# Kernel optimization log

Hardware: AMD Instinct MI355X
Metric: run time of the kernel (lower is better)

The kernel has to match this reference:

```python
import jax, jax.numpy as jnp
import numpy as np

NEG = -1e12


def setup_inputs() -> dict:
    key = jax.random.key(0)
    ks = jax.random.split(key, 6)
    B, S, D, H = 32, 2048, 1024, 1024  # batch, seq, dec/enc dim, hidden
    last_state = jax.random.normal(ks[0], (B, D), dtype=jnp.float32)
    enc_outputs = jax.random.normal(ks[1], (B, S, D), dtype=jnp.float32)
    attn_masks = jax.random.randint(ks[2], (B, S), 0, 2, dtype=jnp.int32)
    W = jax.random.normal(ks[3], (H, 2 * D), dtype=jnp.float32) * 0.02
    b = jax.random.normal(ks[4], (H,), dtype=jnp.float32) * 0.02
    V = jax.random.normal(ks[5], (H,), dtype=jnp.float32)
    return {"last_state": last_state, "enc_outputs": enc_outputs,
            "attn_masks": attn_masks, "W": W, "b": b, "V": V}


def reference(last_state, enc_outputs, attn_masks, W, b, V):
    # Split W to avoid materializing the [B,S,2D] concat:
    # concat([h, e]) @ W.T == h @ Wh.T + e @ We.T
    D = last_state.shape[-1]
    Wh, We = W[:, :D], W[:, D:]
    # hidden part: [B,H], broadcast over seq
    h_part = jnp.einsum('bd,hd->bh', last_state, Wh)  # [B,H]
    e_part = jnp.einsum('bsd,hd->bsh', enc_outputs, We)  # [B,S,H]
    sim = jnp.tanh(h_part[:, None, :] + e_part + b)  # [B,S,H]
    scores = jnp.einsum('bsh,h->bs', sim, V)  # [B,S]
    scores = jnp.where(attn_masks != 1, jnp.float32(NEG), scores)
    attn_weights = jax.nn.softmax(scores, axis=1)  # [B,S]
    context = jnp.einsum('bs,bsd->bd', attn_weights, enc_outputs)  # [B,D]
    return context, attn_weights, scores
```

## Files before the change

### kernel.cpp

```cpp
#include <hip/hip_runtime.h>
#include <math.h>
#include <stdint.h>

#define B_ 32
#define S_ 2048
#define D_ 1024
#define H_ 1024
#define NEGV -1000000000000.0f

typedef __attribute__((ext_vector_type(8))) short bf16x8;
typedef __attribute__((ext_vector_type(8))) _Float16 f16x8;
typedef __attribute__((ext_vector_type(4))) float f32x4;

static __device__ __forceinline__ unsigned short f2bf(float x) {
    union { float f; unsigned u; } v; v.f = x;
    unsigned r = v.u + 0x7FFF + ((v.u >> 16) & 1);
    return (unsigned short)(r >> 16);
}
static __device__ __forceinline__ float bf2f(unsigned short h) {
    union { float f; unsigned u; } v; v.u = ((unsigned)h) << 16; return v.f;
}
static __device__ __forceinline__ unsigned short f2h(float x) {
    _Float16 h = (_Float16)x; unsigned short u;
    __builtin_memcpy(&u, &h, 2); return u;
}
static __device__ __forceinline__ float h2f(unsigned short u) {
    _Float16 h; __builtin_memcpy(&h, &u, 2); return (float)h;
}
static __device__ __forceinline__ float tanh_fast(float x) {
    float e = __expf(2.f * x);
    return 1.f - 2.f / (e + 1.f);
}
static __device__ __forceinline__ void gl_lds16(unsigned short* lds, const unsigned short* g) {
    __builtin_amdgcn_global_load_lds(
        (const __attribute__((address_space(1))) unsigned int*)(const void*)g,
        (__attribute__((address_space(3))) unsigned int*)(void*)lds,
        16, 0, 0);
}

__global__ __launch_bounds__(256) void k_W_f16(const float* __restrict__ W,
                                               unsigned short* __restrict__ out) {
    int idx = blockIdx.x * 256 + threadIdx.x;
    int h = idx >> 7, kc = idx & 127;
    const float* src = W + (size_t)h * (2 * D_) + D_ + kc * 8;
    float4 a = *(const float4*)src;
    float4 c4 = *(const float4*)(src + 4);
    float v[8] = {a.x, a.y, a.z, a.w, c4.x, c4.y, c4.z, c4.w};
    unsigned short t[8];
#pragma unroll
    for (int j = 0; j < 8; ++j) t[j] = f2h(v[j]);
    uint4 w;
    w.x = t[0] | ((unsigned)t[1] << 16); w.y = t[2] | ((unsigned)t[3] << 16);
    w.z = t[4] | ((unsigned)t[5] << 16); w.w = t[6] | ((unsigned)t[7] << 16);
    int g = kc >> 3, cc = kc & 7;
    int dst = g * 64 + ((cc ^ (h & 7)) << 3);
    *(uint4*)(out + (size_t)h * D_ + dst) = w;
}

__global__ __launch_bounds__(256) void k_enc_f16(const float* __restrict__ enc,
                                                 unsigned short* __restrict__ out) {
    size_t gid = (size_t)blockIdx.x * 256 + threadIdx.x;
    size_t row = gid >> 7;
    int kc = (int)(gid & 127);
    const float* src = enc + row * D_ + kc * 8;
    float4 a = *(const float4*)src;
    float4 c4 = *(const float4*)(src + 4);
    float v[8] = {a.x, a.y, a.z, a.w, c4.x, c4.y, c4.z, c4.w};
    unsigned short t[8];
#pragma unroll
    for (int j = 0; j < 8; ++j) t[j] = f2h(v[j]);
    uint4 w;
    w.x = t[0] | ((unsigned)t[1] << 16); w.y = t[2] | ((unsigned)t[3] << 16);
    w.z = t[4] | ((unsigned)t[5] << 16); w.w = t[6] | ((unsigned)t[7] << 16);
    int g = kc >> 3, cc = kc & 7;
    int dst = g * 64 + ((cc ^ ((int)row & 7)) << 3);
    *(uint4*)(out + row * D_ + dst) = w;
}

__global__ __launch_bounds__(256) void k_hpart(const float* __restrict__ ls,
                                               const float* __restrict__ W,
                                               float* __restrict__ hp) {
    int bh = blockIdx.x * 256 + threadIdx.x;
    int b = bh >> 10, h = bh & 1023;
    const float* lsr = ls + b * D_;
    const float* wr  = W + (size_t)h * (2 * D_);
    float acc = 0.f;
#pragma unroll 4
    for (int d = 0; d < D_; d += 4) {
        float4 a = *(const float4*)(lsr + d);
        float4 w = *(const float4*)(wr + d);
        acc += a.x * w.x + a.y * w.y + a.z * w.z + a.w * w.w;
    }
    hp[bh] = acc;
}

__global__ __launch_bounds__(512, 2) void k_scores_f16(
    const unsigned short* __restrict__ ench,
    const unsigned short* __restrict__ Wf16,
    const float* __restrict__ hp, const float* __restrict__ bias,
    const float* __restrict__ V, float* __restrict__ spart)
{
    extern __shared__ unsigned short smem[];
    unsigned short* smemA = smem;
    unsigned short* smemB = smem + 32768;

    const int tid  = threadIdx.x;
    const int lane = tid & 63, wid = tid >> 6;
    const int wm = wid >> 2, wn = wid & 3;
    const int l15 = lane & 15, lhi = lane >> 4;

    const int bid  = blockIdx.x;
    const int wgid = (bid & 7) * 128 + (bid >> 3);
    const int mt = wgid >> 2, nt = wgid & 3;
    const int m0 = mt * 256;
    const int nt256 = nt * 256;
    const int b = m0 >> 11;

    const size_t aoff = (size_t)(m0 + wid * 16 + (lane >> 3)) * D_ + (lane & 7) * 8;
    const size_t boff = (size_t)(nt256 + wid * 16 + (lane >> 3)) * D_ + (lane & 7) * 8;
    const int ldsw = wid * 1024;

    f32x4 acc[8][4];
#pragma unroll
    for (int i = 0; i < 8; ++i)
#pragma unroll
        for (int j = 0; j < 4; ++j)
            acc[i][j] = (f32x4){0.f, 0.f, 0.f, 0.f};

    const int swz = l15 & 7;

#define STAGE_A(SLOT, HALF, KOFS) do {                                              \
    unsigned short* d_ = &smemA[(SLOT) * 16384 + (HALF) * 8192 + ldsw];             \
    const unsigned short* s_ = ench + aoff + (size_t)(HALF) * 131072 + (KOFS);      \
    gl_lds16(d_, s_);                                                               \
    gl_lds16(d_ + 512, s_ + 8192);                                                  \
} while (0)
#define STAGE_B(SLOT, HALF, KOFS) do {                                              \
    unsigned short* d_ = &smemB[(SLOT) * 16384 + (HALF) * 8192 + ldsw];             \
    const unsigned short* s_ = Wf16 + boff + (size_t)(HALF) * 131072 + (KOFS);      \
    gl_lds16(d_, s_);                                                               \
    gl_lds16(d_ + 512, s_ + 8192);                                                  \
} while (0)

#define LDA(AR, CUR, MH, KS) do {                                                   \
    _Pragma("unroll")                                                               \
    for (int fi_ = 0; fi_ < 4; ++fi_) {                                             \
        int row_ = wm * 128 + (MH) * 64 + fi_ * 16 + l15;                           \
        int ch_  = ((KS) * 4 + lhi) ^ swz;                                          \
        AR[fi_] = *(const f16x8*)&smemA[(CUR) * 16384 + row_ * 64 + ch_ * 8];       \
    }                                                                               \
} while (0)
#define LDB(BR, CUR, KS) do {                                                       \
    _Pragma("unroll")                                                               \
    for (int fi_ = 0; fi_ < 4; ++fi_) {                                             \
        int row_ = wn * 64 + fi_ * 16 + l15;                                        \
        int ch_  = ((KS) * 4 + lhi) ^ swz;                                          \
        BR[fi_] = *(const f16x8*)&smemB[(CUR) * 16384 + row_ * 64 + ch_ * 8];       \
    }                                                                               \
} while (0)
#define MFMA16(AR, BR, MH) do {                                                     \
    __builtin_amdgcn_s_setprio(1);                                                  \
    _Pragma("unroll")                                                               \
    for (int fi_ = 0; fi_ < 4; ++fi_)                                               \
    _Pragma("unroll")                                                               \
        for (int fj_ = 0; fj_ < 4; ++fj_)                                           \
            acc[(MH) * 4 + fi_][fj_] = __builtin_amdgcn_mfma_f32_16x16x32_f16(      \
                AR[fi_], BR[fj_], acc[(MH) * 4 + fi_][fj_], 0, 0, 0);               \
    __builtin_amdgcn_s_setprio(0);                                                  \
} while (0)

    STAGE_B(0, 0, 0);
    STAGE_B(0, 1, 0);
    STAGE_A(0, 0, 0);
    STAGE_A(0, 1, 0);
    __syncthreads();

    f16x8 a[4], bk[4];
#pragma unroll 1
    for (int t = 0; t < 16; ++t) {
        const int cur = t & 1, nxt = cur ^ 1;

        if (t < 15) {
            const int kofs = (t + 1) * 64;
            STAGE_B(nxt, 0, kofs);
            STAGE_B(nxt, 1, kofs);
            STAGE_A(nxt, 0, kofs);
            STAGE_A(nxt, 1, kofs);
        }

#pragma unroll
        for (int ks = 0; ks < 2; ++ks) {
            LDB(bk, cur, ks);
            LDA(a, cur, 0, ks);
            MFMA16(a, bk, 0);
            LDA(a, cur, 1, ks);
            MFMA16(a, bk, 1);
        }

        __syncthreads();
    }

    float hb[4], vv[4];
#pragma unroll
    for (int fn = 0; fn < 4; ++fn) {
        int h = nt256 + wn * 64 + fn * 16 + l15;
        hb[fn] = hp[b * H_ + h] + bias[h];
        vv[fn] = V[h];
    }
    float* s_red = (float*)smem;
#pragma unroll
    for (int fm = 0; fm < 8; ++fm)
#pragma unroll
        for (int rg = 0; rg < 4; ++rg) {
            float rs = 0.f;
#pragma unroll
            for (int fn = 0; fn < 4; ++fn)
                rs += tanh_fast(acc[fm][fn][rg] + hb[fn]) * vv[fn];
            rs += __shfl_xor(rs, 1, 16);
            rs += __shfl_xor(rs, 2, 16);
            rs += __shfl_xor(rs, 4, 16);
            rs += __shfl_xor(rs, 8, 16);
            if (l15 == 0)
                s_red[wid * 128 + fm * 16 + lhi * 4 + rg] = rs;
        }
    __syncthreads();
    if (tid < 256) {
        int wmr = tid >> 7, rr = tid & 127;
        float v = s_red[(wmr * 4 + 0) * 128 + rr] + s_red[(wmr * 4 + 1) * 128 + rr]
                + s_red[(wmr * 4 + 2) * 128 + rr] + s_red[(wmr * 4 + 3) * 128 + rr];
        spart[(size_t)nt * 65536 + m0 + tid] = v;
    }
#undef STAGE_A
#undef STAGE_B
#undef LDA
#undef LDB
#undef MFMA16
}

__global__ __launch_bounds__(256) void k_softmax_fold(const float* __restrict__ spart,
                                                      const int* __restrict__ mask,
                                                      float* __restrict__ scores_out,
                                                      float* __restrict__ weights) {
    __shared__ float red[8];
    int b = blockIdx.x, tid = threadIdx.x;
    float vals[8];
    float mx = -INFINITY;
#pragma unroll
    for (int i = 0; i < 8; ++i) {
        int m = b * S_ + tid + i * 256;
        float s = spart[m] + spart[65536 + m] + spart[131072 + m] + spart[196608 + m];
        s = (mask[m] == 1) ? s : NEGV;
        scores_out[m] = s;
        vals[i] = s;
        mx = fmaxf(mx, s);
    }
    for (int off = 32; off; off >>= 1) mx = fmaxf(mx, __shfl_xor(mx, off, 64));
    int wave = tid >> 6;
    if ((tid & 63) == 0) red[wave] = mx;
    __syncthreads();
    mx = fmaxf(fmaxf(red[0], red[1]), fmaxf(red[2], red[3]));
    float sum = 0.f;
#pragma unroll
    for (int i = 0; i < 8; ++i) {
        vals[i] = expf(vals[i] - mx);
        sum += vals[i];
    }
    for (int off = 32; off; off >>= 1) sum += __shfl_xor(sum, off, 64);
    if ((tid & 63) == 0) red[4 + wave] = sum;
    __syncthreads();
    sum = red[4] + red[5] + red[6] + red[7];
    float inv = 1.f / sum;
#pragma unroll
    for (int i = 0; i < 8; ++i)
        weights[b * S_ + tid + i * 256] = vals[i] * inv;
}

__global__ __launch_bounds__(256) void k_ctx_partial_f16(const float* __restrict__ weights,
                                                         const unsigned short* __restrict__ ench,
                                                         float* __restrict__ part) {
    int b = blockIdx.x >> 4;
    int chunk = blockIdx.x & 15;
    int tid = threadIdx.x;
    int d0 = tid * 4;
    int g = d0 >> 6, cc = (d0 >> 3) & 7, o = d0 & 7;
    float4 acc = {0.f, 0.f, 0.f, 0.f};
    int s0 = chunk * 128;
    const float* wrow = weights + b * S_;
    for (int s = s0; s < s0 + 128; ++s) {
        float w = wrow[s];
        if (w != 0.f) {
            int dst = g * 64 + ((cc ^ (s & 7)) << 3) + o;
            ushort4 e = *(const ushort4*)(ench + (size_t)(b * S_ + s) * D_ + dst);
            acc.x += w * h2f(e.x); acc.y += w * h2f(e.y);
            acc.z += w * h2f(e.z); acc.w += w * h2f(e.w);
        }
    }
    *(float4*)(part + (size_t)blockIdx.x * D_ + d0) = acc;
}

__global__ __launch_bounds__(256) void k_ctx_reduce(const float* __restrict__ part,
                                                    float* __restrict__ ctx) {
    int bd = blockIdx.x * 256 + threadIdx.x;
    int b = bd >> 10, d = bd & 1023;
    float acc = 0.f;
#pragma unroll
    for (int c = 0; c < 16; ++c)
        acc += part[(size_t)(b * 16 + c) * D_ + d];
    ctx[bd] = acc;
}

__global__ __launch_bounds__(256) void k_splitW_lin(const float* __restrict__ W,
                                                    unsigned short* __restrict__ hi,
                                                    unsigned short* __restrict__ lo) {
    int idx = blockIdx.x * 256 + threadIdx.x;
    int h = idx >> 7, kc = idx & 127;
    const float* src = W + (size_t)h * (2 * D_) + D_ + kc * 8;
    float4 a = *(const float4*)src;
    float4 c = *(const float4*)(src + 4);
    float v[8] = {a.x, a.y, a.z, a.w, c.x, c.y, c.z, c.w};
    unsigned short th[8], tl[8];
#pragma unroll
    for (int j = 0; j < 8; ++j) {
        th[j] = f2bf(v[j]);
        tl[j] = f2bf(v[j] - bf2f(th[j]));
    }
    uint4 hw, lw;
    hw.x = th[0] | ((unsigned)th[1] << 16); hw.y = th[2] | ((unsigned)th[3] << 16);
    hw.z = th[4] | ((unsigned)th[5] << 16); hw.w = th[6] | ((unsigned)th[7] << 16);
    lw.x = tl[0] | ((unsigned)tl[1] << 16); lw.y = tl[2] | ((unsigned)tl[3] << 16);
    lw.z = tl[4] | ((unsigned)tl[5] << 16); lw.w = tl[6] | ((unsigned)tl[7] << 16);
    *(uint4*)(hi + (size_t)h * D_ + kc * 8) = hw;
    *(uint4*)(lo + (size_t)h * D_ + kc * 8) = lw;
}

__global__ __launch_bounds__(256, 2) void k_scores_mfma_fb(
    const float* __restrict__ enc,
    const unsigned short* __restrict__ Whi,
    const unsigned short* __restrict__ Wlo,
    const float* __restrict__ hp,
    const float* __restrict__ bias,
    const float* __restrict__ V,
    const int* __restrict__ mask,
    float* __restrict__ scores_out)
{
    __shared__ __align__(16) unsigned short smem[4 * 8192];
    unsigned short* sAhi = smem;
    unsigned short* sAlo = smem + 8192;
    unsigned short* sBhi = smem + 16384;
    unsigned short* sBlo = smem + 24576;

    const int tid  = threadIdx.x;
    const int lane = tid & 63, wid = tid >> 6;
    const int wr = wid >> 1, wc = wid & 1;
    const int l15 = lane & 15, lhi = lane >> 4;
    const int m0 = blockIdx.x * 128;
    const int b  = m0 >> 11;

    float rowsum[4][4] = {};
    float4 pa[8];
    uint4  pbh[4], pbl[4];

#define STAGE_LOAD(NB, KB) do {                                            \
    _Pragma("unroll")                                                      \
    for (int i_ = 0; i_ < 4; ++i_) {                                       \
        int c_ = tid + i_ * 256;                                           \
        int r_ = c_ >> 3, kc_ = c_ & 7;                                    \
        const float* ap_ = enc + (size_t)(m0 + r_) * D_ + (KB) * 64 + kc_ * 8; \
        pa[2 * i_]     = *(const float4*)ap_;                              \
        pa[2 * i_ + 1] = *(const float4*)(ap_ + 4);                        \
        size_t bo_ = (size_t)((NB) * 128 + r_) * D_ + (KB) * 64 + kc_ * 8; \
        pbh[i_] = *(const uint4*)(Whi + bo_);                              \
        pbl[i_] = *(const uint4*)(Wlo + bo_);                              \
    }                                                                      \
} while (0)

#define STAGE_WRITE() do {                                                 \
    _Pragma("unroll")                                                      \
    for (int i_ = 0; i_ < 4; ++i_) {                                       \
        int c_ = tid + i_ * 256;                                           \
        int sc_ = c_ ^ ((c_ >> 3) & 7);                                    \
        float vv_[8] = {pa[2*i_].x, pa[2*i_].y, pa[2*i_].z, pa[2*i_].w,    \
                        pa[2*i_+1].x, pa[2*i_+1].y, pa[2*i_+1].z, pa[2*i_+1].w}; \
        unsigned short th_[8], tl_[8];                                     \
        _Pragma("unroll")                                                  \
        for (int j_ = 0; j_ < 8; ++j_) {                                   \
            th_[j_] = f2bf(vv_[j_]);                                       \
            tl_[j_] = f2bf(vv_[j_] - bf2f(th_[j_]));                       \
        }                                                                  \
        uint4 hw_, lw_;                                                    \
        hw_.x = th_[0] | ((unsigned)th_[1] << 16); hw_.y = th_[2] | ((unsigned)th_[3] << 16); \
        hw_.z = th_[4] | ((unsigned)th_[5] << 16); hw_.w = th_[6] | ((unsigned)th_[7] << 16); \
        lw_.x = tl_[0] | ((unsigned)tl_[1] << 16); lw_.y = tl_[2] | ((unsigned)tl_[3] << 16); \
        lw_.z = tl_[4] | ((unsigned)tl_[5] << 16); lw_.w = tl_[6] | ((unsigned)tl_[7] << 16); \
        *(uint4*)&sAhi[sc_ * 8] = hw_;                                     \
        *(uint4*)&sAlo[sc_ * 8] = lw_;                                     \
        *(uint4*)&sBhi[sc_ * 8] = pbh[i_];                                 \
        *(uint4*)&sBlo[sc_ * 8] = pbl[i_];                                 \
    }                                                                      \
} while (0)

    STAGE_LOAD(0, 0);

    for (int nb = 0; nb < 8; ++nb) {
        f32x4 acc[4][4];
#pragma unroll
        for (int i = 0; i < 4; ++i)
#pragma unroll
            for (int j = 0; j < 4; ++j)
                acc[i][j] = (f32x4){0.f, 0.f, 0.f, 0.f};

        for (int kb = 0; kb < 16; ++kb) {
            __syncthreads();
            STAGE_WRITE();
            __syncthreads();
            int nkb = kb + 1, nnb = nb;
            if (nkb == 16) { nkb = 0; nnb = nb + 1; }
            if (nnb < 8) STAGE_LOAD(nnb, nkb);

#pragma unroll
            for (int ks = 0; ks < 2; ++ks) {
                bf16x8 bh[4], bl[4];
#pragma unroll
                for (int fn = 0; fn < 4; ++fn) {
                    int rB = wc * 64 + fn * 16 + l15;
                    int ch = (rB * 8 + ks * 4 + lhi) ^ (rB & 7);
                    bh[fn] = *(const bf16x8*)&sBhi[ch * 8];
                    bl[fn] = *(const bf16x8*)&sBlo[ch * 8];
                }
#pragma unroll
                for (int fm = 0; fm < 4; ++fm) {
                    int rA = wr * 64 + fm * 16 + l15;
                    int ch = (rA * 8 + ks * 4 + lhi) ^ (rA & 7);
                    bf16x8 ah = *(const bf16x8*)&sAhi[ch * 8];
                    bf16x8 al = *(const bf16x8*)&sAlo[ch * 8];
#pragma unroll
                    for (int fn = 0; fn < 4; ++fn) {
                        acc[fm][fn] = __builtin_amdgcn_mfma_f32_16x16x32_bf16(ah, bh[fn], acc[fm][fn], 0, 0, 0);
                        acc[fm][fn] = __builtin_amdgcn_mfma_f32_16x16x32_bf16(ah, bl[fn], acc[fm][fn], 0, 0, 0);
                        acc[fm][fn] = __builtin_amdgcn_mfma_f32_16x16x32_bf16(al, bh[fn], acc[fm][fn], 0, 0, 0);
                    }
                }
            }
        }

        int n0 = nb * 128;
#pragma unroll
        for (int fn = 0; fn < 4; ++fn) {
            int n = n0 + wc * 64 + fn * 16 + l15;
            float hbv = hp[b * H_ + n] + bias[n];
            float vvv = V[n];
#pragma unroll
            for (int fm = 0; fm < 4; ++fm) {
                f32x4 a = acc[fm][fn];
#pragma unroll
                for (int rg = 0; rg < 4; ++rg)
                    rowsum[fm][rg] += tanh_fast(a[rg] + hbv) * vvv;
            }
        }
    }

    __syncthreads();
    float* s_red = (float*)smem;
#pragma unroll
    for (int fm = 0; fm < 4; ++fm)
#pragma unroll
        for (int rg = 0; rg < 4; ++rg) {
            float v = rowsum[fm][rg];
            v += __shfl_xor(v, 1, 16);
            v += __shfl_xor(v, 2, 16);
            v += __shfl_xor(v, 4, 16);
            v += __shfl_xor(v, 8, 16);
            if (l15 == 0)
                s_red[wc * 128 + wr * 64 + fm * 16 + lhi * 4 + rg] = v;
        }
    __syncthreads();
    if (tid < 128) {
        int m = m0 + tid;
        float sc = s_red[tid] + s_red[128 + tid];
        scores_out[m] = (mask[m] == 1) ? sc : NEGV;
    }
#undef STAGE_LOAD
#undef STAGE_WRITE
}

__global__ __launch_bounds__(256) void k_softmax(const float* __restrict__ scores,
                                                 float* __restrict__ weights) {
    __shared__ float red[8];
    int b = blockIdx.x;
    int tid = threadIdx.x;
    const float* srow = scores + b * S_;
    float vals[8];
    float mx = -INFINITY;
#pragma unroll
    for (int i = 0; i < 8; ++i) {
        vals[i] = srow[tid + i * 256];
        mx = fmaxf(mx, vals[i]);
    }
    for (int off = 32; off; off >>= 1) mx = fmaxf(mx, __shfl_xor(mx, off, 64));
    int wave = tid >> 6;
    if ((tid & 63) == 0) red[wave] = mx;
    __syncthreads();
    mx = fmaxf(fmaxf(red[0], red[1]), fmaxf(red[2], red[3]));
    float sum = 0.f;
#pragma unroll
    for (int i = 0; i < 8; ++i) {
        vals[i] = expf(vals[i] - mx);
        sum += vals[i];
    }
    for (int off = 32; off; off >>= 1) sum += __shfl_xor(sum, off, 64);
    if ((tid & 63) == 0) red[4 + wave] = sum;
    __syncthreads();
    sum = red[4] + red[5] + red[6] + red[7];
    float inv = 1.f / sum;
#pragma unroll
    for (int i = 0; i < 8; ++i)
        weights[b * S_ + tid + i * 256] = vals[i] * inv;
}

__global__ __launch_bounds__(256) void k_ctx_partial_f32(const float* __restrict__ weights,
                                                         const float* __restrict__ enc,
                                                         float* __restrict__ part) {
    int b = blockIdx.x >> 4;
    int chunk = blockIdx.x & 15;
    int tid = threadIdx.x;
    int d0 = tid * 4;
    float4 acc = {0.f, 0.f, 0.f, 0.f};
    int s0 = chunk * 128;
    const float* wrow = weights + b * S_;
    for (int s = s0; s < s0 + 128; ++s) {
        float w = wrow[s];
        if (w != 0.f) {
            float4 e = *(const float4*)(enc + (size_t)(b * S_ + s) * D_ + d0);
            acc.x += w * e.x; acc.y += w * e.y; acc.z += w * e.z; acc.w += w * e.w;
        }
    }
    *(float4*)(part + (size_t)blockIdx.x * D_ + d0) = acc;
}

extern "C" void kernel_launch(void* const* d_in, const int* in_sizes, int n_in,
                              void* d_out, int out_size, void* d_ws, size_t ws_size,
                              hipStream_t stream) {
    const float* ls   = (const float*)d_in[0];
    const float* enc  = (const float*)d_in[1];
    const int*   mask = (const int*)d_in[2];
    const float* W    = (const float*)d_in[3];
    const float* bias = (const float*)d_in[4];
    const float* V    = (const float*)d_in[5];

    float* out     = (float*)d_out;
    float* ctx     = out;
    float* weights = out + 32768;
    float* scores  = out + 98304;

    const size_t need = 134217728ull + 2097152ull + 131072ull + 1048576ull + 2097152ull;

    if (ws_size >= need) {
        unsigned short* ench = (unsigned short*)d_ws;
        unsigned short* Wf16 = ench + 67108864;
        float* hp    = (float*)(Wf16 + 1048576);
        float* spart = hp + 32768;
        float* part  = spart + 262144;

        hipFuncSetAttribute((const void*)k_scores_f16,
                            hipFuncAttributeMaxDynamicSharedMemorySize, 131072);

        k_W_f16<<<512, 256, 0, stream>>>(W, Wf16);
        k_enc_f16<<<32768, 256, 0, stream>>>(enc, ench);
        k_hpart<<<128, 256, 0, stream>>>(ls, W, hp);
        k_scores_f16<<<1024, 512, 131072, stream>>>(ench, Wf16, hp, bias, V, spart);
        k_softmax_fold<<<32, 256, 0, stream>>>(spart, mask, scores, weights);
        k_ctx_partial_f16<<<512, 256, 0, stream>>>(weights, ench, part);
        k_ctx_reduce<<<128, 256, 0, stream>>>(part, ctx);
    } else {
        unsigned short* Whi = (unsigned short*)d_ws;
        unsigned short* Wlo = Whi + 1048576;
        float* hp   = (float*)(Wlo + 1048576);
        float* part = hp + 32768;

        k_splitW_lin<<<512, 256, 0, stream>>>(W, Whi, Wlo);
        k_hpart<<<128, 256, 0, stream>>>(ls, W, hp);
        k_scores_mfma_fb<<<512, 256, 0, stream>>>(enc, Whi, Wlo, hp, bias, V, mask, scores);
        k_softmax<<<32, 256, 0, stream>>>(scores, weights);
        k_ctx_partial_f32<<<512, 256, 0, stream>>>(weights, enc, part);
        k_ctx_reduce<<<128, 256, 0, stream>>>(part, ctx);
    }
}
```

Measured before the change: 299.6 us.

## Fuse fp32-to-fp16 encoder conversion into the scores GEMM A-tile load

Drops the separate kernel that converted the whole encoder tensor to fp16 in workspace. The scores GEMM now loads fp32 encoder rows into registers, converts them, and writes swizzled fp16 into LDS, with the global loads issued before the MFMA loop and the LDS writes after it. The context kernel reads the fp32 encoder directly. This removes a 256MB read plus 128MB write pass, but each GEMM block reads fp32 A tiles, doubling A-side load bytes across the four N tiles. It also uses more registers and replaces async global-to-LDS loads with register staging.

```diff
diff --git a/kernel.cpp b/kernel.cpp
--- a/kernel.cpp
+++ b/kernel.cpp
@@ -55,26 +55,6 @@
     int g = kc >> 3, cc = kc & 7;
     int dst = g * 64 + ((cc ^ (h & 7)) << 3);
     *(uint4*)(out + (size_t)h * D_ + dst) = w;
-}
-
-__global__ __launch_bounds__(256) void k_enc_f16(const float* __restrict__ enc,
-                                                 unsigned short* __restrict__ out) {
-    size_t gid = (size_t)blockIdx.x * 256 + threadIdx.x;
-    size_t row = gid >> 7;
-    int kc = (int)(gid & 127);
-    const float* src = enc + row * D_ + kc * 8;
-    float4 a = *(const float4*)src;
-    float4 c4 = *(const float4*)(src + 4);
-    float v[8] = {a.x, a.y, a.z, a.w, c4.x, c4.y, c4.z, c4.w};
-    unsigned short t[8];
-#pragma unroll
-    for (int j = 0; j < 8; ++j) t[j] = f2h(v[j]);
-    uint4 w;
-    w.x = t[0] | ((unsigned)t[1] << 16); w.y = t[2] | ((unsigned)t[3] << 16);
-    w.z = t[4] | ((unsigned)t[5] << 16); w.w = t[6] | ((unsigned)t[7] << 16);
-    int g = kc >> 3, cc = kc & 7;
-    int dst = g * 64 + ((cc ^ ((int)row & 7)) << 3);
-    *(uint4*)(out + row * D_ + dst) = w;
 }
 
 __global__ __launch_bounds__(256) void k_hpart(const float* __restrict__ ls,
@@ -94,8 +74,8 @@
     hp[bh] = acc;
 }
 
-__global__ __launch_bounds__(512, 2) void k_scores_f16(
-    const unsigned short* __restrict__ ench,
+__global__ __launch_bounds__(512, 2) void k_scores_fused(
+    const float* __restrict__ enc,
     const unsigned short* __restrict__ Wf16,
     const float* __restrict__ hp, const float* __restrict__ bias,
     const float* __restrict__ V, float* __restrict__ spart)
@@ -116,7 +96,6 @@
     const int nt256 = nt * 256;
     const int b = m0 >> 11;
 
-    const size_t aoff = (size_t)(m0 + wid * 16 + (lane >> 3)) * D_ + (lane & 7) * 8;
     const size_t boff = (size_t)(nt256 + wid * 16 + (lane >> 3)) * D_ + (lane & 7) * 8;
     const int ldsw = wid * 1024;
 
@@ -129,12 +108,35 @@
 
     const int swz = l15 & 7;
 
-#define STAGE_A(SLOT, HALF, KOFS) do {                                              \
-    unsigned short* d_ = &smemA[(SLOT) * 16384 + (HALF) * 8192 + ldsw];             \
-    const unsigned short* s_ = ench + aoff + (size_t)(HALF) * 131072 + (KOFS);      \
-    gl_lds16(d_, s_);                                                               \
-    gl_lds16(d_ + 512, s_ + 8192);                                                  \
-} while (0)
+    float4 ar0[4], ar1[4];
+
+#define LOAD_A(KOFS) do {                                                           \
+    _Pragma("unroll")                                                               \
+    for (int s_ = 0; s_ < 4; ++s_) {                                                \
+        int p_ = tid + s_ * 512;                                                    \
+        int row_ = p_ >> 3, pc_ = p_ & 7;                                           \
+        const float* ap_ = enc + (size_t)(m0 + row_) * D_ + (KOFS) + pc_ * 8;       \
+        ar0[s_] = *(const float4*)ap_;                                              \
+        ar1[s_] = *(const float4*)(ap_ + 4);                                        \
+    }                                                                               \
+} while (0)
+#define WRITE_A(SLOT) do {                                                          \
+    _Pragma("unroll")                                                               \
+    for (int s_ = 0; s_ < 4; ++s_) {                                                \
+        int p_ = tid + s_ * 512;                                                    \
+        int row_ = p_ >> 3, pc_ = p_ & 7;                                           \
+        float v_[8] = {ar0[s_].x, ar0[s_].y, ar0[s_].z, ar0[s_].w,                  \
+                       ar1[s_].x, ar1[s_].y, ar1[s_].z, ar1[s_].w};                 \
+        unsigned short t_[8];                                                       \
+        _Pragma("unroll")                                                           \
+        for (int j_ = 0; j_ < 8; ++j_) t_[j_] = f2h(v_[j_]);                        \
+        uint4 w_;                                                                   \
+        w_.x = t_[0] | ((unsigned)t_[1] << 16); w_.y = t_[2] | ((unsigned)t_[3] << 16); \
+        w_.z = t_[4] | ((unsigned)t_[5] << 16); w_.w = t_[6] | ((unsigned)t_[7] << 16); \
+        *(uint4*)&smemA[(SLOT) * 16384 + row_ * 64 + ((pc_ ^ (row_ & 7)) << 3)] = w_; \
+    }                                                                               \
+} while (0)
+
 #define STAGE_B(SLOT, HALF, KOFS) do {                                              \
     unsigned short* d_ = &smemB[(SLOT) * 16384 + (HALF) * 8192 + ldsw];             \
     const unsigned short* s_ = Wf16 + boff + (size_t)(HALF) * 131072 + (KOFS);      \
@@ -169,23 +171,22 @@
     __builtin_amdgcn_s_setprio(0);                                                  \
 } while (0)
 
+    LOAD_A(0);
     STAGE_B(0, 0, 0);
     STAGE_B(0, 1, 0);
-    STAGE_A(0, 0, 0);
-    STAGE_A(0, 1, 0);
+    WRITE_A(0);
     __syncthreads();
 
     f16x8 a[4], bk[4];
 #pragma unroll 1
     for (int t = 0; t < 16; ++t) {
         const int cur = t & 1, nxt = cur ^ 1;
+        const int kofs = (t + 1) * 64;
 
         if (t < 15) {
-            const int kofs = (t + 1) * 64;
+            LOAD_A(kofs);
             STAGE_B(nxt, 0, kofs);
             STAGE_B(nxt, 1, kofs);
-            STAGE_A(nxt, 0, kofs);
-            STAGE_A(nxt, 1, kofs);
         }
 
 #pragma unroll
@@ -196,6 +197,8 @@
             LDA(a, cur, 1, ks);
             MFMA16(a, bk, 1);
         }
+
+        if (t < 15) WRITE_A(nxt);
 
         __syncthreads();
     }
@@ -230,7 +233,8 @@
                 + s_red[(wmr * 4 + 2) * 128 + rr] + s_red[(wmr * 4 + 3) * 128 + rr];
         spart[(size_t)nt * 65536 + m0 + tid] = v;
     }
-#undef STAGE_A
+#undef LOAD_A
+#undef WRITE_A
 #undef STAGE_B
 #undef LDA
 #undef LDB
@@ -275,24 +279,21 @@
         weights[b * S_ + tid + i * 256] = vals[i] * inv;
 }
 
-__global__ __launch_bounds__(256) void k_ctx_partial_f16(const float* __restrict__ weights,
-                                                         const unsigned short* __restrict__ ench,
+__global__ __launch_bounds__(256) void k_ctx_partial_f32(const float* __restrict__ weights,
+                                                         const float* __restrict__ enc,
                                                          float* __restrict__ part) {
     int b = blockIdx.x >> 4;
     int chunk = blockIdx.x & 15;
     int tid = threadIdx.x;
     int d0 = tid * 4;
-    int g = d0 >> 6, cc = (d0 >> 3) & 7, o = d0 & 7;
     float4 acc = {0.f, 0.f, 0.f, 0.f};
     int s0 = chunk * 128;
     const float* wrow = weights + b * S_;
     for (int s = s0; s < s0 + 128; ++s) {
         float w = wrow[s];
         if (w != 0.f) {
-            int dst = g * 64 + ((cc ^ (s & 7)) << 3) + o;
-            ushort4 e = *(const ushort4*)(ench + (size_t)(b * S_ + s) * D_ + dst);
-            acc.x += w * h2f(e.x); acc.y += w * h2f(e.y);
-            acc.z += w * h2f(e.z); acc.w += w * h2f(e.w);
+            float4 e = *(const float4*)(enc + (size_t)(b * S_ + s) * D_ + d0);
+            acc.x += w * e.x; acc.y += w * e.y; acc.z += w * e.z; acc.w += w * e.w;
         }
     }
     *(float4*)(part + (size_t)blockIdx.x * D_ + d0) = acc;
@@ -517,26 +518,6 @@
         weights[b * S_ + tid + i * 256] = vals[i] * inv;
 }
 
-__global__ __launch_bounds__(256) void k_ctx_partial_f32(const float* __restrict__ weights,
-                                                         const float* __restrict__ enc,
-                                                         float* __restrict__ part) {
-    int b = blockIdx.x >> 4;
-    int chunk = blockIdx.x & 15;
-    int tid = threadIdx.x;
-    int d0 = tid * 4;
-    float4 acc = {0.f, 0.f, 0.f, 0.f};
-    int s0 = chunk * 128;
-    const float* wrow = weights + b * S_;
-    for (int s = s0; s < s0 + 128; ++s) {
-        float w = wrow[s];
-        if (w != 0.f) {
-            float4 e = *(const float4*)(enc + (size_t)(b * S_ + s) * D_ + d0);
-            acc.x += w * e.x; acc.y += w * e.y; acc.z += w * e.z; acc.w += w * e.w;
-        }
-    }
-    *(float4*)(part + (size_t)blockIdx.x * D_ + d0) = acc;
-}
-
 extern "C" void kernel_launch(void* const* d_in, const int* in_sizes, int n_in,
                               void* d_out, int out_size, void* d_ws, size_t ws_size,
                               hipStream_t stream) {
@@ -552,24 +533,22 @@
     float* weights = out + 32768;
     float* scores  = out + 98304;
 
-    const size_t need = 134217728ull + 2097152ull + 131072ull + 1048576ull + 2097152ull;
+    const size_t need = 2097152ull + 131072ull + 1048576ull + 2097152ull;
 
     if (ws_size >= need) {
-        unsigned short* ench = (unsigned short*)d_ws;
-        unsigned short* Wf16 = ench + 67108864;
+        unsigned short* Wf16 = (unsigned short*)d_ws;
         float* hp    = (float*)(Wf16 + 1048576);
         float* spart = hp + 32768;
         float* part  = spart + 262144;
 
-        hipFuncSetAttribute((const void*)k_scores_f16,
+        hipFuncSetAttribute((const void*)k_scores_fused,
                             hipFuncAttributeMaxDynamicSharedMemorySize, 131072);
 
         k_W_f16<<<512, 256, 0, stream>>>(W, Wf16);
-        k_enc_f16<<<32768, 256, 0, stream>>>(enc, ench);
         k_hpart<<<128, 256, 0, stream>>>(ls, W, hp);
-        k_scores_f16<<<1024, 512, 131072, stream>>>(ench, Wf16, hp, bias, V, spart);
+        k_scores_fused<<<1024, 512, 131072, stream>>>(enc, Wf16, hp, bias, V, spart);
         k_softmax_fold<<<32, 256, 0, stream>>>(spart, mask, scores, weights);
-        k_ctx_partial_f16<<<512, 256, 0, stream>>>(weights, ench, part);
+        k_ctx_partial_f32<<<512, 256, 0, stream>>>(weights, enc, part);
         k_ctx_reduce<<<128, 256, 0, stream>>>(part, ctx);
     } else {
         unsigned short* Whi = (unsigned short*)d_ws;
```

Measured after the change: 256.7 us. 1.17x faster.
